# Kernel optimization log

Measured on AMD Instinct MI355X. Metric: run time of the kernel, lower is better.

## Reference

```python
import jax, jax.numpy as jnp
import numpy as np

K = 128      # scratch_keys_dim
NP = 3       # n_pointers
P = 200      # program_dim
STEPS = 3    # max_program_steps


def _positional_encoding(max_len=50, d=K):
    pos = np.arange(max_len, dtype=np.float32)[:, None]
    div = np.exp(np.arange(0, d, 2, dtype=np.float32) * (-np.log(10000.0) / d))
    pe = np.zeros((max_len, d), dtype=np.float32)
    pe[:, 0::2] = np.sin(pos * div)
    pe[:, 1::2] = np.cos(pos * div)
    return jnp.asarray(pe)


def setup_inputs() -> dict:
    B, I, L, Vin, Vout = 256, 16, 50, 1000, 512
    H = K * NP
    key = jax.random.key(0)
    ks = jax.random.split(key, 8)
    s = 0.05
    return {
        'instructions': jax.random.randint(ks[0], (I, B), 0, Vin),
        'true_actions': jax.random.randint(ks[1], (L, B), 0, Vout),
        'gate_emb': jax.random.normal(ks[2], (Vin, 2), jnp.float32) * s,
        'program_emb': jax.random.normal(ks[3], (Vin, P), jnp.float32) * s,
        'primitive_emb': jax.random.normal(ks[4], (Vin, Vout), jnp.float32) * s,
        'w_ih': jax.random.normal(ks[5], (3 * H, P), jnp.float32) * s,
        'w_hh': jax.random.normal(ks[6], (3 * H, H), jnp.float32) * s,
        'b_ih': jnp.zeros((3 * H,), jnp.float32),
        'b_hh': jnp.zeros((3 * H,), jnp.float32),
        'scratch_keys': _positional_encoding(),
        'init_value': jnp.zeros((Vout,), jnp.float32).at[0].set(1.0),  # one-hot eos
    }


def _gru_cell(x, h, w_ih, w_hh, b_ih, b_hh):
    # torch.nn.GRUCell math
    gi = x @ w_ih.T + b_ih
    gh = h @ w_hh.T + b_hh
    i_r, i_z, i_n = jnp.split(gi, 3, axis=-1)
    h_r, h_z, h_n = jnp.split(gh, 3, axis=-1)
    r = jax.nn.sigmoid(i_r + h_r)
    z = jax.nn.sigmoid(i_z + h_z)
    n = jnp.tanh(i_n + r * h_n)
    return (1.0 - z) * n + z * h


def reference(instructions, true_actions, gate_emb, program_emb, primitive_emb,
              w_ih, w_hh, b_ih, b_hh, scratch_keys, init_value):
    I, B = instructions.shape
    L = true_actions.shape[0]
    keys = scratch_keys[:L]                                    # [L,K], broadcast over batch
    h0 = jnp.tile(scratch_keys[0], (B, NP))                    # [B,3K] init executor hidden
    v0 = jnp.broadcast_to(init_value, (B, L, init_value.shape[0]))  # [B,L,Vout]

    def outer(carry, word):
        h, vals = carry
        gate = jax.nn.softmax(gate_emb[word], axis=-1)         # [B,2] (softmax gate activation)
        program = program_emb[word]                            # [B,P]
        primitive = primitive_emb[word]                        # [B,Vout]
        for _ in range(STEPS):
            read_ptr = h[:, K:2 * K]                           # [B,K]
            write_ptr = h[:, 2 * K:3 * K]                      # [B,K]
            read_attn = jax.nn.softmax(jnp.einsum('bk,lk->bl', read_ptr, keys), axis=-1)
            read_value = jnp.einsum('bl,blv->bv', read_attn, vals)
            # gate-weighted mix of primitive and read value
            new_value = gate[:, :1] * primitive + gate[:, 1:] * read_value   # [B,Vout]
            write_mask = jax.nn.softmax(jnp.einsum('bk,lk->bl', write_ptr, keys), axis=-1)
            vals = write_mask[:, :, None] * new_value[:, None, :] + (1.0 - write_mask[:, :, None]) * vals
            h = _gru_cell(program, h, w_ih, w_hh, b_ih, b_hh)
        return (h, vals), None

    (h, vals), _ = jax.lax.scan(outer, (h0, v0), instructions)
    actions = jnp.transpose(jax.nn.log_softmax(vals, axis=-1), (0, 2, 1))  # [B,Vout,L]
    return actions, true_actions.T
```

## Files before the change

kernel.cpp:

```cpp
#include <hip/hip_runtime.h>
#include <math.h>

#define KK     128
#define HH     384
#define H3     1152
#define PP     200
#define LL     50
#define VV     512
#define BB     256
#define II     16
#define NSTEPS 3

#define NT     640
#define VP2    258
#define KQP    33

#define GH4G   12
#define GIG    13
#define WQ4H_UI (GH4G * 3 * 384 * 4)
#define WQI_UI  (GIG  * 3 * 384 * 4)

__device__ __forceinline__ int dot4(unsigned a, unsigned b, int c) {
    return __builtin_amdgcn_sdot4((int)a, (int)b, c, false);
}
__device__ __forceinline__ int dot8(unsigned a, unsigned b, int c) {
    return __builtin_amdgcn_sdot8((int)a, (int)b, c, false);
}
__device__ __forceinline__ float rcpf(float x) { return __builtin_amdgcn_rcpf(x); }
__device__ __forceinline__ float sigm(float x) { return rcpf(1.f + __expf(-x)); }
__device__ __forceinline__ float tanh_fast(float x) {
    float xc = fminf(fmaxf(x, -15.f), 15.f);
    float t = __expf(2.f * xc);
    return 1.f - 2.f * rcpf(t + 1.f);
}
__device__ __forceinline__ int q8(float x, float sc) {
    int q = (int)rintf(x * sc);
    return q < -127 ? -127 : (q > 127 ? 127 : q);
}
__device__ __forceinline__ int q4(float x, float sc) {
    int q = (int)rintf(x * sc);
    return q < -7 ? -7 : (q > 7 ? 7 : q);
}

__global__ void wmax_reduce(const float* __restrict__ w_hh,
                            const float* __restrict__ w_ih,
                            const float* __restrict__ prog_emb,
                            unsigned* __restrict__ scales)
{
    int idx = blockIdx.x * 256 + threadIdx.x;
    int stride = gridDim.x * 256;
    float mh = 0.f, mi = 0.f, mp = 0.f;
    for (int i = idx; i < HH * H3; i += stride) mh = fmaxf(mh, fabsf(w_hh[i]));
    for (int i = idx; i < PP * H3; i += stride) mi = fmaxf(mi, fabsf(w_ih[i]));
    for (int i = idx; i < 1000 * PP; i += stride) mp = fmaxf(mp, fabsf(prog_emb[i]));
    #pragma unroll
    for (int mm = 32; mm >= 1; mm >>= 1) {
        mh = fmaxf(mh, __shfl_xor(mh, mm, 64));
        mi = fmaxf(mi, __shfl_xor(mi, mm, 64));
        mp = fmaxf(mp, __shfl_xor(mp, mm, 64));
    }
    if ((threadIdx.x & 63) == 0) {
        atomicMax(scales,     __float_as_uint(mh));
        atomicMax(scales + 1, __float_as_uint(mi));
        atomicMax(scales + 2, __float_as_uint(mp));
    }
}

__global__ void pack_weights(const float* __restrict__ w_hh,
                             const float* __restrict__ w_ih,
                             const unsigned* __restrict__ scales,
                             unsigned* __restrict__ wq)
{
    int idx = blockIdx.x * 256 + threadIdx.x;
    if (idx < WQ4H_UI) {
        const float sc = 7.f * rcpf(fmaxf(__uint_as_float(scales[0]), 1e-20f));
        int u4 = idx >> 2, m = idx & 3;
        int g = u4 / (3 * 384);
        int r = u4 - g * (3 * 384);
        int s = r / 384, t = r - s * 384;
        int j = t + 384 * s, k = 32 * g + 8 * m;
        const float* wr = w_hh + (long)j * HH + k;
        unsigned pw = 0;
        #pragma unroll
        for (int e = 0; e < 8; ++e) pw |= ((unsigned)(q4(wr[e], sc) & 0xF)) << (4 * e);
        wq[idx] = pw;
    } else if (idx < WQ4H_UI + WQI_UI) {
        const float sc = 127.f * rcpf(fmaxf(__uint_as_float(scales[1]), 1e-20f));
        int q = idx - WQ4H_UI;
        int u4 = q >> 2, m = q & 3;
        int g = u4 / (3 * 384);
        int r = u4 - g * (3 * 384);
        int s = r / 384, t = r - s * 384;
        int j = t + 384 * s, k = 16 * g + 4 * m;
        unsigned pw = 0;
        #pragma unroll
        for (int e = 0; e < 4; ++e) {
            float w = (k + e < PP) ? w_ih[(long)j * PP + k + e] : 0.f;
            pw |= ((unsigned)(q8(w, sc) & 255)) << (8 * e);
        }
        wq[WQ4H_UI + u4 * 4 + m] = pw;
    }
}

struct __align__(16) Smem {
    float2 vals[LL * VP2];
    unsigned keysq[LL * KQP + 16] __attribute__((aligned(16)));
    unsigned hq4[2][48]     __attribute__((aligned(16)));
    unsigned hq8[2][96]     __attribute__((aligned(16)));
    unsigned progq[56]      __attribute__((aligned(16)));
    float  raw[4][52], wmw[4][52];
    float  rowoff[52];
    float  partial[4 * 52];
};

__global__ __launch_bounds__(NT)
void symop_main(const int* __restrict__ instr,
                const float* __restrict__ gate_emb,
                const float* __restrict__ program_emb,
                const float* __restrict__ primitive_emb,
                const uint4* __restrict__ wqhh,
                const uint4* __restrict__ wqih,
                const unsigned* __restrict__ scales,
                const float* __restrict__ b_ih,
                const float* __restrict__ b_hh,
                const float* __restrict__ keys_g,
                const float* __restrict__ init_value,
                float* __restrict__ out)
{
    __shared__ Smem sm;

    const int tid  = threadIdx.x;
    const int lane = tid & 63;
    const int wid  = tid >> 6;
    const int b    = blockIdx.x;

    const float maxH = fmaxf(__uint_as_float(scales[0]), 1e-20f);
    const float maxI = fmaxf(__uint_as_float(scales[1]), 1e-20f);
    const float maxP = fmaxf(__uint_as_float(scales[2]), 1e-20f);
    const float ghs = maxH * (1.f / 49.f);
    const float gis = maxI * maxP * (1.f / 16129.f);
    const float psc = 127.f * rcpf(maxP);
    const float lsc = 1.f / 16129.f;

    float hcur = 0.f;
    if (tid < HH) hcur = keys_g[tid & 127];
    for (int idx = tid; idx < LL * 32; idx += NT) {
        int l = idx >> 5, kk = idx & 31;
        const float* kr = keys_g + l * KK + 4 * kk;
        unsigned pw = 0;
        #pragma unroll
        for (int e = 0; e < 4; ++e) pw |= ((unsigned)(q8(kr[e], 127.f) & 255)) << (8 * e);
        sm.keysq[l * KQP + kk] = pw;
    }
    if (tid < 96) {
        unsigned pw = 0;
        #pragma unroll
        for (int e = 0; e < 4; ++e) {
            int q = q8(keys_g[(4 * tid + e) & 127], 127.f);
            pw |= ((unsigned)(q & 255)) << (8 * e);
        }
        sm.hq8[0][tid] = pw;
    } else if (tid >= 128 && tid < 128 + 48) {
        int u = tid - 128;
        unsigned pw = 0;
        #pragma unroll
        for (int e = 0; e < 8; ++e) {
            int q = q4(keys_g[(8 * u + e) & 127], 7.f);
            pw |= ((unsigned)(q & 0xF)) << (4 * e);
        }
        sm.hq4[0][u] = pw;
    }
    for (int idx = tid; idx < LL * 256; idx += NT) {
        int l = idx >> 8, c = idx & 255;
        sm.vals[l * VP2 + c] = *(const float2*)(init_value + 2 * c);
    }
    if (tid >= 512 && tid < 512 + 52) {
        int qt = tid - 512;
        int w0 = instr[b];
        const float* pg = program_emb + (long)w0 * PP;
        unsigned pw = 0;
        #pragma unroll
        for (int e = 0; e < 4; ++e) {
            int k = 4 * qt + e;
            float v = (k < PP) ? pg[k] : 0.f;
            pw |= ((unsigned)(q8(v, psc) & 255)) << (8 * e);
        }
        sm.progq[qt] = pw;
    }
    __syncthreads();

    float bh0 = 0, bh1 = 0, bh2 = 0, bi0 = 0, bi1 = 0, bi2 = 0;
    if (tid < HH) {
        bh0 = b_hh[tid]; bh1 = b_hh[tid + HH]; bh2 = b_hh[tid + 2 * HH];
        bi0 = b_ih[tid]; bi1 = b_ih[tid + HH]; bi2 = b_ih[tid + 2 * HH];
    }
    float gic0 = 0, gic1 = 0, gic2 = 0;
    int   gn0 = 0, gn1 = 0, gn2 = 0;

    if (tid < HH) {
        int ia0 = 0, ia1 = 0, ia2 = 0;
        const uint4* wp = wqih + tid;
        #pragma unroll 2
        for (int g = 0; g < GIG; ++g) {
            uint4 w0 = wp[(g * 3 + 0) * 384];
            uint4 w1 = wp[(g * 3 + 1) * 384];
            uint4 w2 = wp[(g * 3 + 2) * 384];
            uint4 hp = *(const uint4*)(sm.progq + 4 * g);
            ia0 = dot4(w0.x, hp.x, ia0); ia0 = dot4(w0.y, hp.y, ia0);
            ia0 = dot4(w0.z, hp.z, ia0); ia0 = dot4(w0.w, hp.w, ia0);
            ia1 = dot4(w1.x, hp.x, ia1); ia1 = dot4(w1.y, hp.y, ia1);
            ia1 = dot4(w1.z, hp.z, ia1); ia1 = dot4(w1.w, hp.w, ia1);
            ia2 = dot4(w2.x, hp.x, ia2); ia2 = dot4(w2.y, hp.y, ia2);
            ia2 = dot4(w2.z, hp.z, ia2); ia2 = dot4(w2.w, hp.w, ia2);
        }
        gic0 = bi0 + (float)ia0 * gis;
        gic1 = bi1 + (float)ia1 * gis;
        gic2 = bi2 + (float)ia2 * gis;
    }

    int par = 0;
    for (int i = 0; i < II; ++i) {
        const int word = instr[i * BB + b];
        for (int t = 0; t < NSTEPS; ++t) {
            if (tid < HH) {
                int ia0 = 0, ia1 = 0, ia2 = 0;
                const uint4* wp = wqhh + tid;
                #pragma unroll 2
                for (int g = 0; g < GH4G; ++g) {
                    uint4 w0 = wp[(g * 3 + 0) * 384];
                    uint4 w1 = wp[(g * 3 + 1) * 384];
                    uint4 w2 = wp[(g * 3 + 2) * 384];
                    uint4 hp = *(const uint4*)(sm.hq4[par] + 4 * g);
                    ia0 = dot8(w0.x, hp.x, ia0); ia0 = dot8(w0.y, hp.y, ia0);
                    ia0 = dot8(w0.z, hp.z, ia0); ia0 = dot8(w0.w, hp.w, ia0);
                    ia1 = dot8(w1.x, hp.x, ia1); ia1 = dot8(w1.y, hp.y, ia1);
                    ia1 = dot8(w1.z, hp.z, ia1); ia1 = dot8(w1.w, hp.w, ia1);
                    ia2 = dot8(w2.x, hp.x, ia2); ia2 = dot8(w2.y, hp.y, ia2);
                    ia2 = dot8(w2.z, hp.z, ia2); ia2 = dot8(w2.w, hp.w, ia2);
                }
                const float gh0 = bh0 + (float)ia0 * ghs;
                const float gh1 = bh1 + (float)ia1 * ghs;
                const float gh2 = bh2 + (float)ia2 * ghs;

                if (i + 1 < II) {
                    const uint4* wi = wqih + tid;
                    if (t == 1) {
                        gn0 = 0; gn1 = 0; gn2 = 0;
                        #pragma unroll 2
                        for (int g = 0; g < 7; ++g) {
                            uint4 w0 = wi[(g * 3 + 0) * 384];
                            uint4 w1 = wi[(g * 3 + 1) * 384];
                            uint4 w2 = wi[(g * 3 + 2) * 384];
                            uint4 hp = *(const uint4*)(sm.progq + 4 * g);
                            gn0 = dot4(w0.x, hp.x, gn0); gn0 = dot4(w0.y, hp.y, gn0);
                            gn0 = dot4(w0.z, hp.z, gn0); gn0 = dot4(w0.w, hp.w, gn0);
                            gn1 = dot4(w1.x, hp.x, gn1); gn1 = dot4(w1.y, hp.y, gn1);
                            gn1 = dot4(w1.z, hp.z, gn1); gn1 = dot4(w1.w, hp.w, gn1);
                            gn2 = dot4(w2.x, hp.x, gn2); gn2 = dot4(w2.y, hp.y, gn2);
                            gn2 = dot4(w2.z, hp.z, gn2); gn2 = dot4(w2.w, hp.w, gn2);
                        }
                    } else if (t == 2) {
                        #pragma unroll 2
                        for (int g = 7; g < GIG; ++g) {
                            uint4 w0 = wi[(g * 3 + 0) * 384];
                            uint4 w1 = wi[(g * 3 + 1) * 384];
                            uint4 w2 = wi[(g * 3 + 2) * 384];
                            uint4 hp = *(const uint4*)(sm.progq + 4 * g);
                            gn0 = dot4(w0.x, hp.x, gn0); gn0 = dot4(w0.y, hp.y, gn0);
                            gn0 = dot4(w0.z, hp.z, gn0); gn0 = dot4(w0.w, hp.w, gn0);
                            gn1 = dot4(w1.x, hp.x, gn1); gn1 = dot4(w1.y, hp.y, gn1);
                            gn1 = dot4(w1.z, hp.z, gn1); gn1 = dot4(w1.w, hp.w, gn1);
                            gn2 = dot4(w2.x, hp.x, gn2); gn2 = dot4(w2.y, hp.y, gn2);
                            gn2 = dot4(w2.z, hp.z, gn2); gn2 = dot4(w2.w, hp.w, gn2);
                        }
                    }
                }

                const float r = sigm(gic0 + gh0);
                const float z = sigm(gic1 + gh1);
                const float n = tanh_fast(gic2 + r * gh2);
                const float hn = (1.f - z) * n + z * hcur;
                hcur = hn;
                int q8v = ((int)rintf(hn * 127.f)) & 255;
                unsigned v1 = (unsigned)q8v | ((unsigned)(__shfl_down(q8v, 1, 64) & 255) << 8);
                unsigned v2 = v1 | ((unsigned)__shfl_down((int)v1, 2, 64) << 16);
                if (!(tid & 3)) sm.hq8[par ^ 1][tid >> 2] = v2;
                int q4v = ((int)rintf(hn * 7.f)) & 0xF;
                unsigned u1 = (unsigned)q4v | ((unsigned)(__shfl_down(q4v, 1, 64) & 0xF) << 4);
                unsigned u2 = u1 | ((unsigned)(__shfl_down((int)u1, 2, 64) & 0xFF) << 8);
                unsigned u4 = u2 | ((unsigned)__shfl_down((int)u2, 4, 64) << 16);
                if (!(tid & 7)) sm.hq4[par ^ 1][tid >> 3] = u4;

                if (t == 2 && i + 1 < II) {
                    gic0 = bi0 + (float)gn0 * gis;
                    gic1 = bi1 + (float)gn1 * gis;
                    gic2 = bi2 + (float)gn2 * gis;
                }
            } else {
                const int w4 = wid - 6;
                float rlog = -1e30f, wlog = -1e30f;
                if (lane < LL) {
                    int ir = 0, iw = 0;
                    const unsigned* kq = sm.keysq + lane * KQP;
                    const uint4* h8r = (const uint4*)(sm.hq8[par] + 32);
                    const uint4* h8w = (const uint4*)(sm.hq8[par] + 64);
                    #pragma unroll
                    for (int o = 0; o < 8; ++o) {
                        uint4 hr = h8r[o], hw = h8w[o];
                        unsigned k0 = kq[4 * o], k1 = kq[4 * o + 1];
                        unsigned k2 = kq[4 * o + 2], k3 = kq[4 * o + 3];
                        ir = dot4(k0, hr.x, ir); ir = dot4(k1, hr.y, ir);
                        ir = dot4(k2, hr.z, ir); ir = dot4(k3, hr.w, ir);
                        iw = dot4(k0, hw.x, iw); iw = dot4(k1, hw.y, iw);
                        iw = dot4(k2, hw.z, iw); iw = dot4(k3, hw.w, iw);
                    }
                    rlog = (float)ir * lsc;
                    wlog = (float)iw * lsc;
                }
                float mr = rlog, mw = wlog;
                #pragma unroll
                for (int mm = 32; mm >= 1; mm >>= 1) {
                    mr = fmaxf(mr, __shfl_xor(mr, mm, 64));
                    mw = fmaxf(mw, __shfl_xor(mw, mm, 64));
                }
                float er = (lane < LL) ? __expf(rlog - mr) : 0.f;
                float ew = (lane < LL) ? __expf(wlog - mw) : 0.f;
                float sr = er, sw = ew;
                #pragma unroll
                for (int mm = 32; mm >= 1; mm >>= 1) {
                    sr += __shfl_xor(sr, mm, 64);
                    sw += __shfl_xor(sw, mm, 64);
                }
                if (lane < LL) {
                    sm.raw[w4][lane] = er * rcpf(sr);
                    sm.wmw[w4][lane] = ew * rcpf(sw);
                }
                const float ge0 = gate_emb[2 * word], ge1 = gate_emb[2 * word + 1];
                const float gmx = fmaxf(ge0, ge1);
                const float e0 = __expf(ge0 - gmx), e1 = __expf(ge1 - gmx);
                const float g0 = e0 * rcpf(e0 + e1), g1 = 1.0f - g0;
                const float* prim = primitive_emb + (long)word * VV;

                const int c = tid - HH;
                float2 pr = *(const float2*)(prim + 2 * c);
                float rv0 = 0.f, rv1 = 0.f;
                #pragma unroll 10
                for (int l = 0; l < LL; ++l) {
                    float2 vv = sm.vals[l * VP2 + c];
                    rv0 = fmaf(sm.raw[w4][l], vv.x, rv0);
                    rv1 = fmaf(sm.raw[w4][l], vv.y, rv1);
                }
                const float nv0 = g0 * pr.x + g1 * rv0;
                const float nv1 = g0 * pr.y + g1 * rv1;
                #pragma unroll 10
                for (int l = 0; l < LL; ++l) {
                    float2 vv = sm.vals[l * VP2 + c];
                    const float w = sm.wmw[w4][l];
                    vv.x = fmaf(w, nv0 - vv.x, vv.x);
                    vv.y = fmaf(w, nv1 - vv.y, vv.y);
                    sm.vals[l * VP2 + c] = vv;
                }
                if (t == 0 && i + 1 < II && tid >= 512 && tid < 512 + 52) {
                    int qt = tid - 512;
                    int wn = instr[(i + 1) * BB + b];
                    const float* pg = program_emb + (long)wn * PP;
                    unsigned pw = 0;
                    #pragma unroll
                    for (int e = 0; e < 4; ++e) {
                        int k = 4 * qt + e;
                        float v = (k < PP) ? pg[k] : 0.f;
                        pw |= ((unsigned)(q8(v, psc) & 255)) << (8 * e);
                    }
                    sm.progq[qt] = pw;
                }
            }
            __syncthreads();
            par ^= 1;
        }
    }

    if (tid < 256) {
        #pragma unroll 5
        for (int l = 0; l < LL; ++l) {
            float2 vv = sm.vals[l * VP2 + tid];
            float e = __expf(vv.x) + __expf(vv.y);
            #pragma unroll
            for (int mm = 32; mm >= 1; mm >>= 1) e += __shfl_xor(e, mm, 64);
            if (lane == 0) sm.partial[wid * 52 + l] = e;
        }
    }
    __syncthreads();
    if (tid < LL) {
        float s = 0.f;
        #pragma unroll
        for (int w = 0; w < 4; ++w) s += sm.partial[w * 52 + tid];
        sm.rowoff[tid] = logf(s);
    }
    __syncthreads();

    if (tid < 256) {
        float* ob0 = out + (long)b * VV * LL + (long)(2 * tid) * LL;
        float* ob1 = ob0 + LL;
        #pragma unroll 5
        for (int l = 0; l < LL; l += 2) {
            float2 va = sm.vals[l * VP2 + tid];
            float2 vb = sm.vals[(l + 1) * VP2 + tid];
            float o0 = sm.rowoff[l], o1 = sm.rowoff[l + 1];
            *(float2*)(ob0 + l) = make_float2(va.x - o0, vb.x - o1);
            *(float2*)(ob1 + l) = make_float2(va.y - o0, vb.y - o1);
        }
    }
}

__global__ void ta_copy(const int* __restrict__ ta, float* __restrict__ out2)
{
    int idx = blockIdx.x * 256 + threadIdx.x;
    if (idx < BB * LL) {
        int b2 = idx / LL, l = idx % LL;
        out2[idx] = (float)ta[l * BB + b2];
    }
}

extern "C" void kernel_launch(void* const* d_in, const int* in_sizes, int n_in,
                              void* d_out, int out_size, void* d_ws, size_t ws_size,
                              hipStream_t stream)
{
    const int*   instr        = (const int*)  d_in[0];
    const int*   true_actions = (const int*)  d_in[1];
    const float* gate_emb     = (const float*)d_in[2];
    const float* program_emb  = (const float*)d_in[3];
    const float* primitive_emb= (const float*)d_in[4];
    const float* w_ih         = (const float*)d_in[5];
    const float* w_hh         = (const float*)d_in[6];
    const float* b_ih         = (const float*)d_in[7];
    const float* b_hh         = (const float*)d_in[8];
    const float* scratch_keys = (const float*)d_in[9];
    const float* init_value   = (const float*)d_in[10];

    unsigned* scales = (unsigned*)d_ws;
    unsigned* wq     = (unsigned*)d_ws + 4;
    const uint4* wqhh = (const uint4*)wq;
    const uint4* wqih = (const uint4*)(wq + WQ4H_UI);

    hipMemsetAsync(scales, 0, 12, stream);
    wmax_reduce<<<256, 256, 0, stream>>>(w_hh, w_ih, program_emb, scales);
    {
        int total = WQ4H_UI + WQI_UI;
        pack_weights<<<(total + 255) / 256, 256, 0, stream>>>(w_hh, w_ih, scales, wq);
    }

    float* out = (float*)d_out;
    float* out_actions = out;
    float* out_ta      = out + (long)BB * VV * LL;

    symop_main<<<BB, NT, 0, stream>>>(instr, gate_emb, program_emb, primitive_emb,
                                      wqhh, wqih, scales, b_ih, b_hh,
                                      scratch_keys, init_value, out_actions);

    ta_copy<<<(BB * LL + 255) / 256, 256, 0, stream>>>(true_actions, out_ta);
}
```

Baseline: 302.7 us.

## Split GRU matvec K-dimension across thread pairs with shuffle reduction

```diff
diff --git a/kernel.cpp b/kernel.cpp
--- a/kernel.cpp
+++ b/kernel.cpp
@@ -11,7 +11,8 @@
 #define II     16
 #define NSTEPS 3
 
-#define NT     640
+#define NT     1024
+#define GRUT   768
 #define VP2    258
 #define KQP    33
 
@@ -133,6 +134,8 @@
     const int lane = tid & 63;
     const int wid  = tid >> 6;
     const int b    = blockIdx.x;
+    const int gl   = tid >> 1;
+    const int koff = tid & 1;
 
     const float maxH = fmaxf(__uint_as_float(scales[0]), 1e-20f);
     const float maxI = fmaxf(__uint_as_float(scales[1]), 1e-20f);
@@ -143,7 +146,7 @@
     const float lsc = 1.f / 16129.f;
 
     float hcur = 0.f;
-    if (tid < HH) hcur = keys_g[tid & 127];
+    if (tid < GRUT) hcur = keys_g[gl & 127];
     for (int idx = tid; idx < LL * 32; idx += NT) {
         int l = idx >> 5, kk = idx & 31;
         const float* kr = keys_g + l * KK + 4 * kk;
@@ -174,8 +177,8 @@
         int l = idx >> 8, c = idx & 255;
         sm.vals[l * VP2 + c] = *(const float2*)(init_value + 2 * c);
     }
-    if (tid >= 512 && tid < 512 + 52) {
-        int qt = tid - 512;
+    if (tid >= GRUT && tid < GRUT + 52) {
+        int qt = tid - GRUT;
         int w0 = instr[b];
         const float* pg = program_emb + (long)w0 * PP;
         unsigned pw = 0;
@@ -190,21 +193,21 @@
     __syncthreads();
 
     float bh0 = 0, bh1 = 0, bh2 = 0, bi0 = 0, bi1 = 0, bi2 = 0;
-    if (tid < HH) {
-        bh0 = b_hh[tid]; bh1 = b_hh[tid + HH]; bh2 = b_hh[tid + 2 * HH];
-        bi0 = b_ih[tid]; bi1 = b_ih[tid + HH]; bi2 = b_ih[tid + 2 * HH];
+    if (tid < GRUT) {
+        bh0 = b_hh[gl]; bh1 = b_hh[gl + HH]; bh2 = b_hh[gl + 2 * HH];
+        bi0 = b_ih[gl]; bi1 = b_ih[gl + HH]; bi2 = b_ih[gl + 2 * HH];
     }
     float gic0 = 0, gic1 = 0, gic2 = 0;
     int   gn0 = 0, gn1 = 0, gn2 = 0;
 
-    if (tid < HH) {
+    if (tid < GRUT) {
         int ia0 = 0, ia1 = 0, ia2 = 0;
-        const uint4* wp = wqih + tid;
-        #pragma unroll 2
-        for (int g = 0; g < GIG; ++g) {
-            uint4 w0 = wp[(g * 3 + 0) * 384];
-            uint4 w1 = wp[(g * 3 + 1) * 384];
-            uint4 w2 = wp[(g * 3 + 2) * 384];
+        const uint4* wi = wqih + gl;
+        const int gs = koff ? 7 : 0, ge = koff ? GIG : 7;
+        for (int g = gs; g < ge; ++g) {
+            uint4 w0 = wi[(g * 3 + 0) * 384];
+            uint4 w1 = wi[(g * 3 + 1) * 384];
+            uint4 w2 = wi[(g * 3 + 2) * 384];
             uint4 hp = *(const uint4*)(sm.progq + 4 * g);
             ia0 = dot4(w0.x, hp.x, ia0); ia0 = dot4(w0.y, hp.y, ia0);
             ia0 = dot4(w0.z, hp.z, ia0); ia0 = dot4(w0.w, hp.w, ia0);
@@ -213,6 +216,9 @@
             ia2 = dot4(w2.x, hp.x, ia2); ia2 = dot4(w2.y, hp.y, ia2);
             ia2 = dot4(w2.z, hp.z, ia2); ia2 = dot4(w2.w, hp.w, ia2);
         }
+        ia0 += __shfl_xor(ia0, 1, 64);
+        ia1 += __shfl_xor(ia1, 1, 64);
+        ia2 += __shfl_xor(ia2, 1, 64);
         gic0 = bi0 + (float)ia0 * gis;
         gic1 = bi1 + (float)ia1 * gis;
         gic2 = bi2 + (float)ia2 * gis;
@@ -222,11 +228,13 @@
     for (int i = 0; i < II; ++i) {
         const int word = instr[i * BB + b];
         for (int t = 0; t < NSTEPS; ++t) {
-            if (tid < HH) {
+            if (tid < GRUT) {
                 int ia0 = 0, ia1 = 0, ia2 = 0;
-                const uint4* wp = wqhh + tid;
+                const uint4* wp = wqhh + gl;
+                const int gb = koff * 6;
                 #pragma unroll 2
-                for (int g = 0; g < GH4G; ++g) {
+                for (int gg = 0; gg < 6; ++gg) {
+                    const int g = gb + gg;
                     uint4 w0 = wp[(g * 3 + 0) * 384];
                     uint4 w1 = wp[(g * 3 + 1) * 384];
                     uint4 w2 = wp[(g * 3 + 2) * 384];
@@ -238,41 +246,54 @@
                     ia2 = dot8(w2.x, hp.x, ia2); ia2 = dot8(w2.y, hp.y, ia2);
                     ia2 = dot8(w2.z, hp.z, ia2); ia2 = dot8(w2.w, hp.w, ia2);
                 }
+                ia0 += __shfl_xor(ia0, 1, 64);
+                ia1 += __shfl_xor(ia1, 1, 64);
+                ia2 += __shfl_xor(ia2, 1, 64);
                 const float gh0 = bh0 + (float)ia0 * ghs;
                 const float gh1 = bh1 + (float)ia1 * ghs;
                 const float gh2 = bh2 + (float)ia2 * ghs;
 
                 if (i + 1 < II) {
-                    const uint4* wi = wqih + tid;
+                    const uint4* wi = wqih + gl;
                     if (t == 1) {
                         gn0 = 0; gn1 = 0; gn2 = 0;
-                        #pragma unroll 2
-                        for (int g = 0; g < 7; ++g) {
-                            uint4 w0 = wi[(g * 3 + 0) * 384];
-                            uint4 w1 = wi[(g * 3 + 1) * 384];
-                            uint4 w2 = wi[(g * 3 + 2) * 384];
-                            uint4 hp = *(const uint4*)(sm.progq + 4 * g);
-                            gn0 = dot4(w0.x, hp.x, gn0); gn0 = dot4(w0.y, hp.y, gn0);
-                            gn0 = dot4(w0.z, hp.z, gn0); gn0 = dot4(w0.w, hp.w, gn0);
-                            gn1 = dot4(w1.x, hp.x, gn1); gn1 = dot4(w1.y, hp.y, gn1);
-                            gn1 = dot4(w1.z, hp.z, gn1); gn1 = dot4(w1.w, hp.w, gn1);
-                            gn2 = dot4(w2.x, hp.x, gn2); gn2 = dot4(w2.y, hp.y, gn2);
-                            gn2 = dot4(w2.z, hp.z, gn2); gn2 = dot4(w2.w, hp.w, gn2);
+                        if (!koff) {
+                            #pragma unroll 2
+                            for (int g = 0; g < 7; ++g) {
+                                uint4 w0 = wi[(g * 3 + 0) * 384];
+                                uint4 w1 = wi[(g * 3 + 1) * 384];
+                                uint4 w2 = wi[(g * 3 + 2) * 384];
+                                uint4 hp = *(const uint4*)(sm.progq + 4 * g);
+                                gn0 = dot4(w0.x, hp.x, gn0); gn0 = dot4(w0.y, hp.y, gn0);
+                                gn0 = dot4(w0.z, hp.z, gn0); gn0 = dot4(w0.w, hp.w, gn0);
+                                gn1 = dot4(w1.x, hp.x, gn1); gn1 = dot4(w1.y, hp.y, gn1);
+                                gn1 = dot4(w1.z, hp.z, gn1); gn1 = dot4(w1.w, hp.w, gn1);
+                                gn2 = dot4(w2.x, hp.x, gn2); gn2 = dot4(w2.y, hp.y, gn2);
+                                gn2 = dot4(w2.z, hp.z, gn2); gn2 = dot4(w2.w, hp.w, gn2);
+                            }
                         }
                     } else if (t == 2) {
-                        #pragma unroll 2
-                        for (int g = 7; g < GIG; ++g) {
-                            uint4 w0 = wi[(g * 3 + 0) * 384];
-                            uint4 w1 = wi[(g * 3 + 1) * 384];
-                            uint4 w2 = wi[(g * 3 + 2) * 384];
-                            uint4 hp = *(const uint4*)(sm.progq + 4 * g);
-                            gn0 = dot4(w0.x, hp.x, gn0); gn0 = dot4(w0.y, hp.y, gn0);
-                            gn0 = dot4(w0.z, hp.z, gn0); gn0 = dot4(w0.w, hp.w, gn0);
-                            gn1 = dot4(w1.x, hp.x, gn1); gn1 = dot4(w1.y, hp.y, gn1);
-                            gn1 = dot4(w1.z, hp.z, gn1); gn1 = dot4(w1.w, hp.w, gn1);
-                            gn2 = dot4(w2.x, hp.x, gn2); gn2 = dot4(w2.y, hp.y, gn2);
-                            gn2 = dot4(w2.z, hp.z, gn2); gn2 = dot4(w2.w, hp.w, gn2);
+                        if (koff) {
+                            #pragma unroll 2
+                            for (int g = 7; g < GIG; ++g) {
+                                uint4 w0 = wi[(g * 3 + 0) * 384];
+                                uint4 w1 = wi[(g * 3 + 1) * 384];
+                                uint4 w2 = wi[(g * 3 + 2) * 384];
+                                uint4 hp = *(const uint4*)(sm.progq + 4 * g);
+                                gn0 = dot4(w0.x, hp.x, gn0); gn0 = dot4(w0.y, hp.y, gn0);
+                                gn0 = dot4(w0.z, hp.z, gn0); gn0 = dot4(w0.w, hp.w, gn0);
+                                gn1 = dot4(w1.x, hp.x, gn1); gn1 = dot4(w1.y, hp.y, gn1);
+                                gn1 = dot4(w1.z, hp.z, gn1); gn1 = dot4(w1.w, hp.w, gn1);
+                                gn2 = dot4(w2.x, hp.x, gn2); gn2 = dot4(w2.y, hp.y, gn2);
+                                gn2 = dot4(w2.z, hp.z, gn2); gn2 = dot4(w2.w, hp.w, gn2);
+                            }
                         }
+                        const int f0 = gn0 + __shfl_xor(gn0, 1, 64);
+                        const int f1 = gn1 + __shfl_xor(gn1, 1, 64);
+                        const int f2 = gn2 + __shfl_xor(gn2, 1, 64);
+                        gic0 = bi0 + (float)f0 * gis;
+                        gic1 = bi1 + (float)f1 * gis;
+                        gic2 = bi2 + (float)f2 * gis;
                     }
                 }
 
@@ -282,22 +303,16 @@
                 const float hn = (1.f - z) * n + z * hcur;
                 hcur = hn;
                 int q8v = ((int)rintf(hn * 127.f)) & 255;
-                unsigned v1 = (unsigned)q8v | ((unsigned)(__shfl_down(q8v, 1, 64) & 255) << 8);
-                unsigned v2 = v1 | ((unsigned)__shfl_down((int)v1, 2, 64) << 16);
-                if (!(tid & 3)) sm.hq8[par ^ 1][tid >> 2] = v2;
+                unsigned v1 = (unsigned)q8v | ((unsigned)(__shfl_down(q8v, 2, 64) & 255) << 8);
+                unsigned v2 = v1 | ((unsigned)__shfl_down((int)v1, 4, 64) << 16);
+                if (!(tid & 7)) sm.hq8[par ^ 1][tid >> 3] = v2;
                 int q4v = ((int)rintf(hn * 7.f)) & 0xF;
-                unsigned u1 = (unsigned)q4v | ((unsigned)(__shfl_down(q4v, 1, 64) & 0xF) << 4);
-                unsigned u2 = u1 | ((unsigned)(__shfl_down((int)u1, 2, 64) & 0xFF) << 8);
-                unsigned u4 = u2 | ((unsigned)__shfl_down((int)u2, 4, 64) << 16);
-                if (!(tid & 7)) sm.hq4[par ^ 1][tid >> 3] = u4;
-
-                if (t == 2 && i + 1 < II) {
-                    gic0 = bi0 + (float)gn0 * gis;
-                    gic1 = bi1 + (float)gn1 * gis;
-                    gic2 = bi2 + (float)gn2 * gis;
-                }
+                unsigned u1 = (unsigned)q4v | ((unsigned)(__shfl_down(q4v, 2, 64) & 0xF) << 4);
+                unsigned u2 = u1 | ((unsigned)(__shfl_down((int)u1, 4, 64) & 0xFF) << 8);
+                unsigned u4 = u2 | ((unsigned)__shfl_down((int)u2, 8, 64) << 16);
+                if (!(tid & 15)) sm.hq4[par ^ 1][tid >> 4] = u4;
             } else {
-                const int w4 = wid - 6;
+                const int w4 = wid - 12;
                 float rlog = -1e30f, wlog = -1e30f;
                 if (lane < LL) {
                     int ir = 0, iw = 0;
@@ -341,7 +356,7 @@
                 const float g0 = e0 * rcpf(e0 + e1), g1 = 1.0f - g0;
                 const float* prim = primitive_emb + (long)word * VV;
 
-                const int c = tid - HH;
+                const int c = tid - GRUT;
                 float2 pr = *(const float2*)(prim + 2 * c);
                 float rv0 = 0.f, rv1 = 0.f;
                 #pragma unroll 10
@@ -360,8 +375,8 @@
                     vv.y = fmaf(w, nv1 - vv.y, vv.y);
                     sm.vals[l * VP2 + c] = vv;
                 }
-                if (t == 0 && i + 1 < II && tid >= 512 && tid < 512 + 52) {
-                    int qt = tid - 512;
+                if (t == 0 && i + 1 < II && tid < GRUT + 52) {
+                    int qt = tid - GRUT;
                     int wn = instr[(i + 1) * BB + b];
                     const float* pg = program_emb + (long)wn * PP;
                     unsigned pw = 0;
```

New measurement: 343.3 us. 1.13x slower.
